# Optimization experiments

Measured on AMD Instinct MI355X. Metric: run time of the kernel, lower is better.

The kernel has to match this reference:

```python
import jax, jax.numpy as jnp
import numpy as np


def conv2d_same(x, w, b):
    # x: (B,C,H,W), w: (O,I,3,3) -> 3x3 'same' conv, stride 1
    y = jax.lax.conv_general_dilated(
        x, w, window_strides=(1, 1), padding=((1, 1), (1, 1)),
        dimension_numbers=("NCHW", "OIHW", "NCHW"))
    return y + b[None, :, None, None]


def setup_inputs() -> dict:
    key = jax.random.key(0)
    ks = jax.random.split(key, 7)
    B, F, E, H, W = 16, 64, 16, 64, 64
    fan2d = F * 9
    state = jax.random.normal(ks[0], (B, F, H, W), dtype=jnp.float32)
    pre_w = jax.random.normal(ks[1], (F, F, 3, 3), dtype=jnp.float32) / np.sqrt(fan2d)
    pre_b = jax.random.normal(ks[2], (F,), dtype=jnp.float32) * 0.01
    attn_w = jax.random.normal(ks[3], (E, F, 3, 3), dtype=jnp.float32) / np.sqrt(fan2d)
    attn_b = jax.random.normal(ks[4], (E,), dtype=jnp.float32) * 0.01
    c3_w = jax.random.normal(ks[5], (F, F), dtype=jnp.float32) / np.sqrt(F)
    c3_b = jax.random.normal(ks[6], (F,), dtype=jnp.float32) * 0.01
    return {"state": state, "pre_w": pre_w, "pre_b": pre_b,
            "attn_w": attn_w, "attn_b": attn_b, "c3_w": c3_w, "c3_b": c3_b}


def reference(state, pre_w, pre_b, attn_w, attn_b, c3_w, c3_b):
    # pre_conv + relu
    x = jax.nn.relu(conv2d_same(state, pre_w, pre_b))
    # visattn_conv + sigmoid -> (B,E,H,W)
    attn = jax.nn.sigmoid(conv2d_same(x, attn_w, attn_b))
    # einsum 'bfyx,beyx->bfeyx'
    x5 = state[:, :, None, :, :] * attn[:, None, :, :, :]  # (B,F,E,H,W)
    # Conv3d kernel (1,1,1) with padding (0,1,1): zero-pad H,W by 1,
    # then pointwise linear over F. Output spatial dims become (E, H+2, W+2).
    x5 = jnp.pad(x5, ((0, 0), (0, 0), (0, 0), (1, 1), (1, 1)))
    y = jnp.einsum("of,bfeyx->boeyx", c3_w, x5) + c3_b[None, :, None, None, None]
    y = jax.nn.relu(y)
    # permute (0,2,1,3,4) then mean over last two dims -> (B,E,F)
    out = jnp.mean(y, axis=(-1, -2)).transpose(0, 2, 1)
    return out, attn
```

## Files before the change

kernel.cpp:

```cpp
#include <hip/hip_runtime.h>
#include <math.h>

constexpr int B = 16, F = 64, E = 16, H = 64, W = 64;
constexpr int XP = 66;
constexpr int CP = 72;
constexpr int SPP = 68;
constexpr int YSTRIDE = XP * F;

typedef __bf16 bf16x8 __attribute__((ext_vector_type(8)));
typedef __bf16 bf16x4 __attribute__((ext_vector_type(4)));
typedef float f32x16 __attribute__((ext_vector_type(16)));
typedef float f32x4 __attribute__((ext_vector_type(4)));

__global__ __launch_bounds__(256) void prep_kernel(
    const float* __restrict__ state, const float* __restrict__ pre_w,
    const float* __restrict__ attn_w, const float* __restrict__ c3_w,
    __bf16* __restrict__ xTs, __bf16* __restrict__ wA1f,
    __bf16* __restrict__ wA2f, __bf16* __restrict__ wT3bf,
    float* __restrict__ out0)
{
    __shared__ float s_t[64][68];
    const int blk = blockIdx.x;
    const int tid = threadIdx.x;

    if (blk < 1024) {
        const int b = blk >> 6, y = blk & 63;
        {
            int c = tid >> 2, x0 = (tid & 3) * 16;
            const float* src = state + ((size_t)(b * F + c) * H + y) * W + x0;
            #pragma unroll
            for (int q = 0; q < 4; ++q)
                *(float4*)&s_t[c][x0 + 4 * q] = *(const float4*)(src + 4 * q);
        }
        __syncthreads();
        __bf16* dst = xTs + (size_t)(b * H + y) * YSTRIDE;
        #pragma unroll
        for (int i = 0; i < 2; ++i) {
            int t = tid + i * 256;
            int x = t >> 3, cg = t & 7;
            bf16x8 v;
            #pragma unroll
            for (int j = 0; j < 8; ++j) v[j] = (__bf16)s_t[cg * 8 + j][x];
            *(bf16x8*)(dst + (x + 1) * F + cg * 8) = v;
        }
        if (tid < 16) {
            int bd = tid >> 3, cg = tid & 7;
            bf16x8 z = {};
            *(bf16x8*)(dst + (bd ? 65 : 0) * F + cg * 8) = z;
        }
    } else if (blk < 1168) {
        int idx = (blk - 1024) * 256 + tid;
        {
            int j = idx & 7, n = (idx >> 3) & 31, kh = (idx >> 8) & 1;
            int mt = (idx >> 9) & 1, cq = (idx >> 10) & 3, t9 = idx >> 12;
            int o = mt * 32 + n, c = cq * 16 + kh * 8 + j;
            wA1f[idx] = (__bf16)pre_w[(o * 64 + c) * 9 + t9];
        }
        if (idx < 9216) {
            int j = idx & 7, n16 = (idx >> 3) & 15, quad = (idx >> 7) & 3;
            int cq = (idx >> 9) & 1, t9 = idx >> 10;
            int c = cq * 32 + quad * 8 + j;
            wA2f[idx] = (__bf16)attn_w[(n16 * 64 + c) * 9 + t9];
        }
        if (idx < 4096) {
            int j = idx & 7, n = (idx >> 3) & 31, kh = (idx >> 8) & 1;
            int mt = (idx >> 9) & 1, cq = idx >> 10;
            wT3bf[idx] = (__bf16)c3_w[(mt * 32 + n) * 64 + cq * 16 + kh * 8 + j];
        }
    } else {
        int idx = (blk - 1168) * 256 + tid;
        float4 z = {0.f, 0.f, 0.f, 0.f};
        *(float4*)(out0 + idx * 4) = z;
    }
}

__global__ __launch_bounds__(256, 2) void mega_kernel(
    const __bf16* __restrict__ xTs, const __bf16* __restrict__ wA1f,
    const __bf16* __restrict__ wA2f, const __bf16* __restrict__ wT3bf,
    const float* __restrict__ pre_b, const float* __restrict__ attn_b,
    const float* __restrict__ c3_b,
    float* __restrict__ attn_out, float* __restrict__ out)
{
    __shared__ __align__(16) char smem[63616];
    const int b = blockIdx.y, yp = blockIdx.x;
    const int tid = threadIdx.x;
    const int wave = tid >> 6, lane = tid & 63;
    const int y0 = yp * 2;

    __bf16* s_in = (__bf16*)smem;
    __bf16* sxo  = (__bf16*)smem;
    __bf16* s_sp = (__bf16*)(smem + 38016);
    float (*s_attn)[64][16] = (float(*)[64][16])(smem + 55424);

    for (int t = tid; t < 6 * XP * 8; t += 256) {
        int r = t / (XP * 8), rem = t - r * (XP * 8);
        int x = rem >> 3, cg = rem & 7;
        int yy = y0 - 2 + r;
        bf16x8 v = {};
        if (yy >= 0 && yy < H)
            v = *(const bf16x8*)(xTs + (size_t)(b * H + yy) * YSTRIDE + x * F + cg * 8);
        *(bf16x8*)(s_in + (r * XP + x) * CP + cg * 8) = v;
    }
    __syncthreads();

    const int n = lane & 31, kh = lane >> 5;
    const int mt = wave & 1, nt = wave >> 1;

    bf16x8 spA[4];
    #pragma unroll
    for (int cq = 0; cq < 4; ++cq)
        spA[cq] = *(const bf16x8*)(wT3bf + cq * 1024 + mt * 512 + kh * 256 + n * 8);

    const int yr = y0 - 1 + wave;
    const bool valid = (yr >= 0 && yr < H);
    f32x16 acc[4] = {};
    if (valid) {
        #pragma unroll
        for (int dy = 0; dy < 3; ++dy) {
            #pragma unroll
            for (int dx = 0; dx < 3; ++dx) {
                const int t9 = dy * 3 + dx;
                const __bf16* bB = s_in + ((wave + dy) * XP + (n + dx)) * CP + kh * 8;
                const __bf16* aB = wA1f + t9 * 4096 + kh * 256 + n * 8;
                #pragma unroll
                for (int cq = 0; cq < 4; ++cq) {
                    bf16x8 a0 = *(const bf16x8*)(aB + cq * 1024);
                    bf16x8 a1 = *(const bf16x8*)(aB + cq * 1024 + 512);
                    bf16x8 b0 = *(const bf16x8*)(bB + cq * 16);
                    bf16x8 b1 = *(const bf16x8*)(bB + 32 * CP + cq * 16);
                    acc[0] = __builtin_amdgcn_mfma_f32_32x32x16_bf16(a0, b0, acc[0], 0, 0, 0);
                    acc[1] = __builtin_amdgcn_mfma_f32_32x32x16_bf16(a0, b1, acc[1], 0, 0, 0);
                    acc[2] = __builtin_amdgcn_mfma_f32_32x32x16_bf16(a1, b0, acc[2], 0, 0, 0);
                    acc[3] = __builtin_amdgcn_mfma_f32_32x32x16_bf16(a1, b1, acc[3], 0, 0, 0);
                }
            }
        }
    }

    f32x16 accsp[2] = {};
    #pragma unroll
    for (int rr = 0; rr < 2; ++rr)
        #pragma unroll
        for (int cq = 0; cq < 4; ++cq) {
            bf16x8 bb = *(const bf16x8*)(s_in + ((2 + rr) * XP + nt * 32 + n + 1) * CP
                                         + cq * 16 + kh * 8);
            accsp[rr] = __builtin_amdgcn_mfma_f32_32x32x16_bf16(spA[cq], bb, accsp[rr], 0, 0, 0);
        }

    __syncthreads();

    {
        __bf16* orow = sxo + wave * XP * CP;
        #pragma unroll
        for (int mt2 = 0; mt2 < 2; ++mt2)
            #pragma unroll
            for (int g = 0; g < 4; ++g) {
                int o0 = mt2 * 32 + kh * 4 + g * 8;
                f32x4 b4 = *(const f32x4*)(pre_b + o0);
                bf16x4 v0 = {}, v1 = {};
                if (valid) {
                    #pragma unroll
                    for (int r = 0; r < 4; ++r) {
                        v0[r] = (__bf16)fmaxf(acc[mt2 * 2 + 0][g * 4 + r] + b4[r], 0.f);
                        v1[r] = (__bf16)fmaxf(acc[mt2 * 2 + 1][g * 4 + r] + b4[r], 0.f);
                    }
                }
                *(bf16x4*)(orow + (n + 1) * CP + o0) = v0;
                *(bf16x4*)(orow + (n + 33) * CP + o0) = v1;
            }
        const int p = nt * 32 + n;
        #pragma unroll
        for (int rr = 0; rr < 2; ++rr)
            #pragma unroll
            for (int g = 0; g < 4; ++g)
                #pragma unroll
                for (int r = 0; r < 4; ++r) {
                    int o = mt * 32 + kh * 4 + g * 8 + r;
                    s_sp[(rr * 64 + o) * SPP + p] = (__bf16)accsp[rr][g * 4 + r];
                }
        if (tid < 64) {
            int r = tid >> 4, bd = (tid >> 3) & 1, cg = tid & 7;
            bf16x8 z = {};
            *(bf16x8*)(sxo + (r * XP + (bd ? 65 : 0)) * CP + cg * 8) = z;
        }
    }
    __syncthreads();

    {
        const int rw = wave >> 1, nt2 = wave & 1;
        const int n16 = lane & 15, quad = lane >> 4;
        f32x4 acc2[2] = {};
        #pragma unroll
        for (int dy = 0; dy < 3; ++dy)
            #pragma unroll
            for (int dx = 0; dx < 3; ++dx) {
                const int t9 = dy * 3 + dx;
                #pragma unroll
                for (int cq = 0; cq < 2; ++cq) {
                    bf16x8 a = *(const bf16x8*)(wA2f + ((t9 * 2 + cq) * 4 + quad) * 128
                                                + n16 * 8);
                    #pragma unroll
                    for (int i = 0; i < 2; ++i) {
                        const __bf16* bp = sxo +
                            ((rw + dy) * XP + (nt2 * 32 + i * 16 + n16 + dx)) * CP
                            + quad * 8 + cq * 32;
                        acc2[i] = __builtin_amdgcn_mfma_f32_16x16x32_bf16(
                            a, *(const bf16x8*)bp, acc2[i], 0, 0, 0);
                    }
                }
            }
        #pragma unroll
        for (int i = 0; i < 2; ++i) {
            int x = nt2 * 32 + i * 16 + n16;
            #pragma unroll
            for (int r = 0; r < 4; ++r) {
                int e = quad * 4 + r;
                float val = acc2[i][r] + attn_b[e];
                float sg = 1.f / (1.f + __expf(-val));
                attn_out[((size_t)(b * E + e) * H + (y0 + rw)) * W + x] = sg;
                s_attn[rw][x][e] = sg;
            }
        }
    }
    __syncthreads();

    {
        const int o = tid & 63, eg = tid >> 6;
        const float cb = c3_b[o];
        float accl[4] = {0.f, 0.f, 0.f, 0.f};
        #pragma unroll
        for (int rr = 0; rr < 2; ++rr) {
            const __bf16* spr = s_sp + (rr * 64 + o) * SPP;
            #pragma unroll 2
            for (int pb = 0; pb < 8; ++pb) {
                bf16x8 sp8 = *(const bf16x8*)(spr + pb * 8);
                #pragma unroll
                for (int k = 0; k < 8; ++k) {
                    float spf = (float)sp8[k];
                    f32x4 a4 = *(const f32x4*)&s_attn[rr][pb * 8 + k][eg * 4];
                    #pragma unroll
                    for (int i = 0; i < 4; ++i)
                        accl[i] += fmaxf(fmaf(a4[i], spf, cb), 0.f);
                }
            }
        }
        const float border = (yp == 0) ? 260.f * fmaxf(cb, 0.f) : 0.f;
        #pragma unroll
        for (int i = 0; i < 4; ++i) {
            int e = eg * 4 + i;
            atomicAdd(&out[(b * E + e) * F + o], (accl[i] + border) * (1.f / 4356.f));
        }
    }
}

extern "C" void kernel_launch(void* const* d_in, const int* in_sizes, int n_in,
                              void* d_out, int out_size, void* d_ws, size_t ws_size,
                              hipStream_t stream) {
    (void)in_sizes; (void)n_in; (void)out_size; (void)ws_size;
    const float* state  = (const float*)d_in[0];
    const float* pre_w  = (const float*)d_in[1];
    const float* pre_b  = (const float*)d_in[2];
    const float* attn_w = (const float*)d_in[3];
    const float* attn_b = (const float*)d_in[4];
    const float* c3_w   = (const float*)d_in[5];
    const float* c3_b   = (const float*)d_in[6];

    float* out      = (float*)d_out;
    float* attn_out = out + B * E * F;

    char* ws = (char*)d_ws;
    constexpr size_t XT_BYTES = (size_t)B * H * YSTRIDE * 2;
    __bf16* xTs   = (__bf16*)ws;
    __bf16* wA1f  = (__bf16*)(ws + XT_BYTES);
    __bf16* wA2f  = (__bf16*)(ws + XT_BYTES + 73728);
    __bf16* wT3bf = (__bf16*)(ws + XT_BYTES + 73728 + 18432);

    prep_kernel<<<1184, 256, 0, stream>>>(state, pre_w, attn_w, c3_w,
                                          xTs, wA1f, wA2f, wT3bf, out);
    mega_kernel<<<dim3(H / 2, B), 256, 0, stream>>>(xTs, wA1f, wA2f, wT3bf,
                                                    pre_b, attn_b, c3_b,
                                                    attn_out, out);
}
```

Before: 106.0 us.

## Split each row-pair block into two x-halves to double grid and occupancy

Each fused conv block now covers half the image width (32 columns plus halo) instead of the full row, so the grid doubles to 64x16 blocks. The shared-memory footprint drops from about 62KB to 34KB, and launch bounds go from 2 to 4 blocks per CU, with the MFMA tiling per wave remapped to match. The aim is to fill the MI355X's CUs better and hide latency with more resident waves. In exchange, each block reloads a wider halo relative to its useful work and issues more atomic adds to the output.

Result: slower. 108.2 us (+2.1%).

```diff
diff --git a/kernel.cpp b/kernel.cpp
--- a/kernel.cpp
+++ b/kernel.cpp
@@ -3,8 +3,9 @@
 
 constexpr int B = 16, F = 64, E = 16, H = 64, W = 64;
 constexpr int XP = 66;
-constexpr int CP = 72;
-constexpr int SPP = 68;
+constexpr int XW = 36;
+constexpr int CPL = 72;
+constexpr int SPPL = 40;
 constexpr int YSTRIDE = XP * F;
 
 typedef __bf16 bf16x8 __attribute__((ext_vector_type(8)));
@@ -74,44 +75,41 @@
     }
 }
 
-__global__ __launch_bounds__(256, 2) void mega_kernel(
+__global__ __launch_bounds__(256, 4) void mega_kernel(
     const __bf16* __restrict__ xTs, const __bf16* __restrict__ wA1f,
     const __bf16* __restrict__ wA2f, const __bf16* __restrict__ wT3bf,
     const float* __restrict__ pre_b, const float* __restrict__ attn_b,
     const float* __restrict__ c3_b,
     float* __restrict__ attn_out, float* __restrict__ out)
 {
-    __shared__ __align__(16) char smem[63616];
-    const int b = blockIdx.y, yp = blockIdx.x;
+    __shared__ __align__(16) char smem[35072];
+    const int b = blockIdx.y;
+    const int yp = blockIdx.x >> 1, xh = blockIdx.x & 1;
     const int tid = threadIdx.x;
     const int wave = tid >> 6, lane = tid & 63;
-    const int y0 = yp * 2;
+    const int y0 = yp * 2, xh0 = xh * 32;
 
     __bf16* s_in = (__bf16*)smem;
     __bf16* sxo  = (__bf16*)smem;
-    __bf16* s_sp = (__bf16*)(smem + 38016);
-    float (*s_attn)[64][16] = (float(*)[64][16])(smem + 55424);
-
-    for (int t = tid; t < 6 * XP * 8; t += 256) {
-        int r = t / (XP * 8), rem = t - r * (XP * 8);
-        int x = rem >> 3, cg = rem & 7;
+    __bf16* s_sp = (__bf16*)(smem + 20736);
+    float (*s_attn)[32][16] = (float(*)[32][16])(smem + 30976);
+
+    for (int t = tid; t < 6 * XW * 8; t += 256) {
+        int r = t / (XW * 8), rem = t - r * (XW * 8);
+        int l = rem >> 3, cg = rem & 7;
         int yy = y0 - 2 + r;
+        int xc = xh0 - 1 + l;
         bf16x8 v = {};
-        if (yy >= 0 && yy < H)
-            v = *(const bf16x8*)(xTs + (size_t)(b * H + yy) * YSTRIDE + x * F + cg * 8);
-        *(bf16x8*)(s_in + (r * XP + x) * CP + cg * 8) = v;
+        if ((unsigned)yy < (unsigned)H && (unsigned)xc < (unsigned)XP)
+            v = *(const bf16x8*)(xTs + (size_t)(b * H + yy) * YSTRIDE + xc * F + cg * 8);
+        *(bf16x8*)(s_in + (r * XW + l) * CPL + cg * 8) = v;
     }
     __syncthreads();
 
     const int n = lane & 31, kh = lane >> 5;
-    const int mt = wave & 1, nt = wave >> 1;
-
-    bf16x8 spA[4];
-    #pragma unroll
-    for (int cq = 0; cq < 4; ++cq)
-        spA[cq] = *(const bf16x8*)(wT3bf + cq * 1024 + mt * 512 + kh * 256 + n * 8);
-
-    const int yr = y0 - 1 + wave;
+
+    const int r1 = wave;
+    const int yr = y0 - 1 + r1;
     const bool valid = (yr >= 0 && yr < H);
     f32x16 acc[4] = {};
     if (valid) {
@@ -120,76 +118,70 @@
             #pragma unroll
             for (int dx = 0; dx < 3; ++dx) {
                 const int t9 = dy * 3 + dx;
-                const __bf16* bB = s_in + ((wave + dy) * XP + (n + dx)) * CP + kh * 8;
                 const __bf16* aB = wA1f + t9 * 4096 + kh * 256 + n * 8;
+                const __bf16* bB = s_in + ((r1 + dy) * XW + (n + dx)) * CPL + kh * 8;
                 #pragma unroll
                 for (int cq = 0; cq < 4; ++cq) {
                     bf16x8 a0 = *(const bf16x8*)(aB + cq * 1024);
                     bf16x8 a1 = *(const bf16x8*)(aB + cq * 1024 + 512);
                     bf16x8 b0 = *(const bf16x8*)(bB + cq * 16);
-                    bf16x8 b1 = *(const bf16x8*)(bB + 32 * CP + cq * 16);
+                    bf16x8 b1 = *(const bf16x8*)(bB + 2 * CPL + cq * 16);
                     acc[0] = __builtin_amdgcn_mfma_f32_32x32x16_bf16(a0, b0, acc[0], 0, 0, 0);
-                    acc[1] = __builtin_amdgcn_mfma_f32_32x32x16_bf16(a0, b1, acc[1], 0, 0, 0);
-                    acc[2] = __builtin_amdgcn_mfma_f32_32x32x16_bf16(a1, b0, acc[2], 0, 0, 0);
+                    acc[1] = __builtin_amdgcn_mfma_f32_32x32x16_bf16(a1, b0, acc[1], 0, 0, 0);
+                    acc[2] = __builtin_amdgcn_mfma_f32_32x32x16_bf16(a0, b1, acc[2], 0, 0, 0);
                     acc[3] = __builtin_amdgcn_mfma_f32_32x32x16_bf16(a1, b1, acc[3], 0, 0, 0);
                 }
             }
         }
     }
 
-    f32x16 accsp[2] = {};
+    const int mt_s = wave & 1, rr_s = wave >> 1;
+    f32x16 accsp = {};
     #pragma unroll
-    for (int rr = 0; rr < 2; ++rr)
-        #pragma unroll
-        for (int cq = 0; cq < 4; ++cq) {
-            bf16x8 bb = *(const bf16x8*)(s_in + ((2 + rr) * XP + nt * 32 + n + 1) * CP
-                                         + cq * 16 + kh * 8);
-            accsp[rr] = __builtin_amdgcn_mfma_f32_32x32x16_bf16(spA[cq], bb, accsp[rr], 0, 0, 0);
-        }
-
+    for (int cq = 0; cq < 4; ++cq) {
+        bf16x8 a  = *(const bf16x8*)(wT3bf + cq * 1024 + mt_s * 512 + kh * 256 + n * 8);
+        bf16x8 bb = *(const bf16x8*)(s_in + ((2 + rr_s) * XW + n + 2) * CPL
+                                     + cq * 16 + kh * 8);
+        accsp = __builtin_amdgcn_mfma_f32_32x32x16_bf16(a, bb, accsp, 0, 0, 0);
+    }
     __syncthreads();
 
     {
-        __bf16* orow = sxo + wave * XP * CP;
-        #pragma unroll
-        for (int mt2 = 0; mt2 < 2; ++mt2)
-            #pragma unroll
-            for (int g = 0; g < 4; ++g) {
-                int o0 = mt2 * 32 + kh * 4 + g * 8;
-                f32x4 b4 = *(const f32x4*)(pre_b + o0);
-                bf16x4 v0 = {}, v1 = {};
-                if (valid) {
-                    #pragma unroll
-                    for (int r = 0; r < 4; ++r) {
-                        v0[r] = (__bf16)fmaxf(acc[mt2 * 2 + 0][g * 4 + r] + b4[r], 0.f);
-                        v1[r] = (__bf16)fmaxf(acc[mt2 * 2 + 1][g * 4 + r] + b4[r], 0.f);
+        __bf16* orow = sxo + r1 * XW * CPL;
+        #pragma unroll
+        for (int t = 0; t < 2; ++t) {
+            const bool edge = (t == 0) ? (xh == 0 && n == 0)
+                                       : (xh == 1 && n == 31);
+            const bool wr = valid && !edge;
+            #pragma unroll
+            for (int mt2 = 0; mt2 < 2; ++mt2)
+                #pragma unroll
+                for (int g = 0; g < 4; ++g) {
+                    int o0 = mt2 * 32 + kh * 4 + g * 8;
+                    f32x4 b4 = *(const f32x4*)(pre_b + o0);
+                    bf16x4 v0 = {};
+                    if (wr) {
+                        #pragma unroll
+                        for (int r = 0; r < 4; ++r)
+                            v0[r] = (__bf16)fmaxf(acc[t * 2 + mt2][g * 4 + r] + b4[r], 0.f);
                     }
-                }
-                *(bf16x4*)(orow + (n + 1) * CP + o0) = v0;
-                *(bf16x4*)(orow + (n + 33) * CP + o0) = v1;
-            }
-        const int p = nt * 32 + n;
-        #pragma unroll
-        for (int rr = 0; rr < 2; ++rr)
-            #pragma unroll
-            for (int g = 0; g < 4; ++g)
-                #pragma unroll
-                for (int r = 0; r < 4; ++r) {
-                    int o = mt * 32 + kh * 4 + g * 8 + r;
-                    s_sp[(rr * 64 + o) * SPP + p] = (__bf16)accsp[rr][g * 4 + r];
-                }
-        if (tid < 64) {
-            int r = tid >> 4, bd = (tid >> 3) & 1, cg = tid & 7;
-            bf16x8 z = {};
-            *(bf16x8*)(sxo + (r * XP + (bd ? 65 : 0)) * CP + cg * 8) = z;
-        }
+                    *(bf16x4*)(orow + (2 * t + n) * CPL + o0) = v0;
+                }
+        }
+        #pragma unroll
+        for (int g = 0; g < 4; ++g)
+            #pragma unroll
+            for (int r = 0; r < 4; ++r) {
+                int o = mt_s * 32 + kh * 4 + g * 8 + r;
+                s_sp[(rr_s * 64 + o) * SPPL + n] = (__bf16)accsp[g * 4 + r];
+            }
     }
     __syncthreads();
 
     {
-        const int rw = wave >> 1, nt2 = wave & 1;
+        const int rw = wave >> 1, xq = wave & 1;
         const int n16 = lane & 15, quad = lane >> 4;
-        f32x4 acc2[2] = {};
+        f32x4 acc2 = {};
         #pragma unroll
         for (int dy = 0; dy < 3; ++dy)
             #pragma unroll
@@ -199,27 +191,20 @@
                 for (int cq = 0; cq < 2; ++cq) {
                     bf16x8 a = *(const bf16x8*)(wA2f + ((t9 * 2 + cq) * 4 + quad) * 128
                                                 + n16 * 8);
-                    #pragma unroll
-                    for (int i = 0; i < 2; ++i) {
-                        const __bf16* bp = sxo +
-                            ((rw + dy) * XP + (nt2 * 32 + i * 16 + n16 + dx)) * CP
-                            + quad * 8 + cq * 32;
-                        acc2[i] = __builtin_amdgcn_mfma_f32_16x16x32_bf16(
-                            a, *(const bf16x8*)bp, acc2[i], 0, 0, 0);
-                    }
-                }
-            }
-        #pragma unroll
-        for (int i = 0; i < 2; ++i) {
-            int x = nt2 * 32 + i * 16 + n16;
-            #pragma unroll
-            for (int r = 0; r < 4; ++r) {
-                int e = quad * 4 + r;
-                float val = acc2[i][r] + attn_b[e];
-                float sg = 1.f / (1.f + __expf(-val));
-                attn_out[((size_t)(b * E + e) * H + (y0 + rw)) * W + x] = sg;
-                s_attn[rw][x][e] = sg;
-            }
+                    const __bf16* bp = sxo +
+                        ((rw + dy) * XW + (xq * 16 + n16 + dx)) * CPL + quad * 8 + cq * 32;
+                    acc2 = __builtin_amdgcn_mfma_f32_16x16x32_bf16(
+                        a, *(const bf16x8*)bp, acc2, 0, 0, 0);
+                }
+            }
+        const int xl = xq * 16 + n16;
+        #pragma unroll
+        for (int r = 0; r < 4; ++r) {
+            int e = quad * 4 + r;
+            float val = acc2[r] + attn_b[e];
+            float sg = 1.f / (1.f + __expf(-val));
+            attn_out[((size_t)(b * E + e) * H + (y0 + rw)) * W + xh0 + xl] = sg;
+            s_attn[rw][xl][e] = sg;
         }
     }
     __syncthreads();
@@ -230,9 +215,9 @@
         float accl[4] = {0.f, 0.f, 0.f, 0.f};
         #pragma unroll
         for (int rr = 0; rr < 2; ++rr) {
-            const __bf16* spr = s_sp + (rr * 64 + o) * SPP;
-            #pragma unroll 2
-            for (int pb = 0; pb < 8; ++pb) {
+            const __bf16* spr = s_sp + (rr * 64 + o) * SPPL;
+            #pragma unroll
+            for (int pb = 0; pb < 4; ++pb) {
                 bf16x8 sp8 = *(const bf16x8*)(spr + pb * 8);
                 #pragma unroll
                 for (int k = 0; k < 8; ++k) {
@@ -244,7 +229,7 @@
                 }
             }
         }
-        const float border = (yp == 0) ? 260.f * fmaxf(cb, 0.f) : 0.f;
+        const float border = (blockIdx.x == 0) ? 260.f * fmaxf(cb, 0.f) : 0.f;
         #pragma unroll
         for (int i = 0; i < 4; ++i) {
             int e = eg * 4 + i;
@@ -277,7 +262,7 @@
 
     prep_kernel<<<1184, 256, 0, stream>>>(state, pre_w, attn_w, c3_w,
                                           xTs, wA1f, wA2f, wT3bf, out);
-    mega_kernel<<<dim3(H / 2, B), 256, 0, stream>>>(xTs, wA1f, wA2f, wT3bf,
-                                                    pre_b, attn_b, c3_b,
-                                                    attn_out, out);
+    mega_kernel<<<dim3(64, B), 256, 0, stream>>>(xTs, wA1f, wA2f, wT3bf,
+                                                 pre_b, attn_b, c3_b,
+                                                 attn_out, out);
 }
```
